# Performance work log

Measured on AMD Instinct MI355X. Metric: run time of the kernel, lower is better.

The kernel has to match this reference:

```python
import jax, jax.numpy as jnp
import numpy as np

N = 500000
D = 256
B = 1024  # number of graphs / segments


def setup_inputs() -> dict:
    key = jax.random.key(0)
    k1, k2, k3, k4 = jax.random.split(key, 4)
    x = jax.random.normal(k1, (N, D), dtype=jnp.float32)
    batch = jnp.sort(jax.random.randint(k2, (N,), 0, B))
    W1 = jax.random.normal(k3, (D, D // 2), dtype=jnp.float32) * (1.0 / np.sqrt(D))
    b1 = jnp.zeros((D // 2,), dtype=jnp.float32)
    W2 = jax.random.normal(k4, (D // 2, 1), dtype=jnp.float32) * (1.0 / np.sqrt(D // 2))
    b2 = jnp.zeros((1,), dtype=jnp.float32)
    return {"x": x, "batch": batch, "W1": W1, "b1": b1, "W2": W2, "b2": b2}


def _segment_mean(vals, seg, num_segments):
    # torch_scatter scatter_mean: sum / count (0 for empty segments)
    s = jax.ops.segment_sum(vals, seg, num_segments=num_segments)
    cnt = jax.ops.segment_sum(jnp.ones((vals.shape[0],), vals.dtype), seg,
                              num_segments=num_segments)
    return s / jnp.maximum(cnt, 1.0)[:, None]


def reference(x, batch, W1, b1, W2, b2):
    n = x.shape[0]
    # attention MLP -> (N, 1)
    h = jax.nn.relu(x @ W1 + b1)
    w = h @ W2 + b2
    # global max-shifted exp (as in source: w - w.max())
    w = jnp.exp(w - jnp.max(w))
    # denom = scatter_mean(w, batch)[batch] * N
    mean_w = _segment_mean(w, batch, B)            # (B, 1)
    denom = mean_w[batch] * jnp.float32(n)          # (N, 1)
    # pooled = scatter_mean(w * x / (denom + 1e-8), batch)
    pooled = _segment_mean(w * x / (denom + 1e-8), batch, B)  # (B, D)
    return pooled
```

## Files before the change

kernel.cpp:

```cpp
#include <hip/hip_runtime.h>
#include <math.h>

typedef float f32x4 __attribute__((ext_vector_type(4)));
typedef __attribute__((ext_vector_type(8))) _Float16 f16x8;
typedef __attribute__((ext_vector_type(4))) _Float16 f16x4;

#define DD 256
#define DH 128
#define NSPLIT 2
#define TROWS 64

__global__ void ap_setup(const float* __restrict__ W1, _Float16* __restrict__ w1f,
                         const int* __restrict__ batch, int* __restrict__ start,
                         int nrows, int bseg) {
  const int bid = blockIdx.x;
  if (bid < 16) {
    int t = bid * 256 + threadIdx.x;
    int l = t & 63;
    int tile = t >> 6;
    int kt = tile >> 3, nt = tile & 7;
    int kbase = kt * 32 + (l >> 4) * 8;
    int col = nt * 16 + (l & 15);
#pragma unroll
    for (int j = 0; j < 8; ++j) {
      w1f[t * 8 + j] = (_Float16)W1[(kbase + j) * DH + col];
    }
  } else {
    int i = (bid - 16) * 256 + threadIdx.x;
    if (i >= nrows) return;
    int c = batch[i];
    int p = (i == 0) ? -1 : batch[i - 1];
    for (int b = p + 1; b <= c; ++b) start[b] = i;
    if (i == nrows - 1) {
      for (int b = c + 1; b <= bseg; ++b) start[b] = nrows;
    }
  }
}

__global__ __launch_bounds__(512, 1)
void ap_fused(const float* __restrict__ x, const _Float16* __restrict__ w1f,
              const float* __restrict__ b1, const float* __restrict__ W2,
              const float* __restrict__ b2, const int* __restrict__ start,
              float* __restrict__ pooledPart, float* __restrict__ mPart,
              float* __restrict__ swPart, int nrows) {
  __shared__ __align__(16) _Float16 xsh[2][TROWS * 256];
  __shared__ float praw[2][4][TROWS];
  __shared__ float swArr[8];

  const int tid = threadIdx.x;
  const int wv = tid >> 6;
  const int np = wv & 3;
  const int rgp = wv >> 2;
  const int l = tid & 63;
  const int l15 = l & 15, lhi = l >> 4;

  const int bi = blockIdx.x;
  const int b = bi >> 1;
  const int q = bi & (NSPLIT - 1);
  const int s0 = start[b], e0 = start[b + 1];
  const int cnt = e0 - s0;
  const int L = (cnt + NSPLIT - 1) >> 1;
  const int s = s0 + q * L;
  int pe = s + L;
  if (pe > e0) pe = e0;
  const int e = pe;
  const int ce = (e > 0) ? (e - 1) : 0;

  f16x8 Breg[16];
#pragma unroll
  for (int kt = 0; kt < 8; ++kt) {
#pragma unroll
    for (int nt2 = 0; nt2 < 2; ++nt2) {
      Breg[kt * 2 + nt2] =
          *((const f16x8*)w1f + (size_t)(kt * 8 + np * 2 + nt2) * 64 + l);
    }
  }

  float b1f[2], w2f[2];
#pragma unroll
  for (int nt2 = 0; nt2 < 2; ++nt2) {
    const int idx = (np * 2 + nt2) * 16 + l15;
    b1f[nt2] = b1[idx];
    w2f[nt2] = W2[idx];
  }
  const float bb = *b2;
  const float NI = -__builtin_inff();

  f32x4 accp = {0.f, 0.f, 0.f, 0.f};
  float m = NI;
  float swv = 0.f;

  f32x4 xcol[8], xnext[8];
#pragma unroll
  for (int i = 0; i < 8; ++i) {
    int grow = s + wv * 8 + i;
    if (grow > ce) grow = ce;
    if (grow < 0) grow = 0;
    xcol[i] = *(const f32x4*)(x + (size_t)grow * DD + l * 4);
  }
#pragma unroll
  for (int i = 0; i < 8; ++i) {
    const int R = wv * 8 + i;
    const int gp = l ^ ((R & 7) << 1);
    f16x4 h4;
#pragma unroll
    for (int j = 0; j < 4; ++j) h4[j] = (_Float16)xcol[i][j];
    *(f16x4*)(xsh[0] + (size_t)(R * 64 + gp) * 4) = h4;
  }
  __syncthreads();

  int buf = 0;
  for (int t0 = s; t0 < e; t0 += TROWS) {
    const bool hasNext = (t0 + TROWS < e);

    if (hasNext) {
#pragma unroll
      for (int i = 0; i < 8; ++i) {
        int grow = t0 + TROWS + wv * 8 + i;
        if (grow > ce) grow = ce;
        xnext[i] = *(const f32x4*)(x + (size_t)grow * DD + l * 4);
      }
    }

    f32x4 acc[2][2];
#pragma unroll
    for (int rg2 = 0; rg2 < 2; ++rg2)
#pragma unroll
      for (int nt2 = 0; nt2 < 2; ++nt2) acc[rg2][nt2] = f32x4{0.f, 0.f, 0.f, 0.f};
#pragma unroll
    for (int kt = 0; kt < 8; ++kt) {
#pragma unroll
      for (int rg2 = 0; rg2 < 2; ++rg2) {
        const int Rr = rgp * 32 + rg2 * 16 + l15;
        const int gp = (kt * 8 + lhi * 2) ^ ((Rr & 7) << 1);
        const f16x8 ah = *(const f16x8*)(xsh[buf] + (size_t)(Rr * 64 + gp) * 4);
        acc[rg2][0] =
            __builtin_amdgcn_mfma_f32_16x16x32_f16(ah, Breg[kt * 2 + 0], acc[rg2][0], 0, 0, 0);
        acc[rg2][1] =
            __builtin_amdgcn_mfma_f32_16x16x32_f16(ah, Breg[kt * 2 + 1], acc[rg2][1], 0, 0, 0);
      }
    }

    float pr[2][4];
#pragma unroll
    for (int rg2 = 0; rg2 < 2; ++rg2) {
#pragma unroll
      for (int r = 0; r < 4; ++r) {
        float t = fmaxf(acc[rg2][0][r] + b1f[0], 0.f) * w2f[0] +
                  fmaxf(acc[rg2][1][r] + b1f[1], 0.f) * w2f[1];
        pr[rg2][r] = t;
      }
    }
#pragma unroll
    for (int mm = 1; mm < 16; mm <<= 1) {
#pragma unroll
      for (int rg2 = 0; rg2 < 2; ++rg2)
#pragma unroll
        for (int r = 0; r < 4; ++r) pr[rg2][r] += __shfl_xor(pr[rg2][r], mm, 64);
    }
    if (l15 == 0) {
#pragma unroll
      for (int rg2 = 0; rg2 < 2; ++rg2)
#pragma unroll
        for (int r = 0; r < 4; ++r)
          praw[buf][np][rgp * 32 + rg2 * 16 + lhi * 4 + r] = pr[rg2][r];
    }

    if (hasNext) {
#pragma unroll
      for (int i = 0; i < 8; ++i) {
        const int R = wv * 8 + i;
        const int gp = l ^ ((R & 7) << 1);
        f16x4 h4;
#pragma unroll
        for (int j = 0; j < 4; ++j) h4[j] = (_Float16)xnext[i][j];
        *(f16x4*)(xsh[buf ^ 1] + (size_t)(R * 64 + gp) * 4) = h4;
      }
    }

    __syncthreads();

    const float tot = (t0 + l < e)
                          ? (praw[buf][0][l] + praw[buf][1][l] +
                             praw[buf][2][l] + praw[buf][3][l] + bb)
                          : NI;
    float tv = tot;
#pragma unroll
    for (int mm = 1; mm < 64; mm <<= 1) tv = fmaxf(tv, __shfl_xor(tv, mm, 64));
    const float nm = fmaxf(m, tv);
    const float factor = expf(m - nm);
    m = nm;
    accp *= factor;
    swv *= factor;

#pragma unroll
    for (int i = 0; i < 8; ++i) {
      const int R = wv * 8 + i;
      const float wi = expf(__shfl(tot, R, 64) - m);
      swv += wi;
      accp += wi * xcol[i];
    }
#pragma unroll
    for (int i = 0; i < 8; ++i) xcol[i] = xnext[i];
    buf ^= 1;
  }

  __syncthreads();
  float* pooled = (float*)xsh;
  *(f32x4*)(pooled + (size_t)(wv * 256 + l * 4)) = accp;
  if (l == 0) swArr[wv] = swv;
  __syncthreads();
  if (tid < 64) {
    float sum_w = 0.f;
#pragma unroll
    for (int p = 0; p < 8; ++p) sum_w += swArr[p];
    const f32x4* pw = (const f32x4*)pooled;
    f32x4 v = ((pw[0 * 64 + tid] + pw[1 * 64 + tid]) +
               (pw[2 * 64 + tid] + pw[3 * 64 + tid]));
    f32x4 w = ((pw[4 * 64 + tid] + pw[5 * 64 + tid]) +
               (pw[6 * 64 + tid] + pw[7 * 64 + tid]));
    *(f32x4*)(pooledPart + (size_t)bi * DD + tid * 4) = v + w;
    if (tid == 0) { mPart[bi] = m; swPart[bi] = sum_w; }
  }
}

__global__ __launch_bounds__(64)
void ap_final(const float* __restrict__ pooledPart, const float* __restrict__ mPart,
              const float* __restrict__ swPart, const int* __restrict__ start,
              float* __restrict__ out, int nrows) {
  const int b = blockIdx.x;
  const int tid = threadIdx.x;
  const float NI = -__builtin_inff();
  float mq[NSPLIT];
#pragma unroll
  for (int qv = 0; qv < NSPLIT; ++qv) mq[qv] = mPart[b * NSPLIT + qv];
  float m_f = NI;
#pragma unroll
  for (int qv = 0; qv < NSPLIT; ++qv) m_f = fmaxf(m_f, mq[qv]);
  float fac[NSPLIT];
  float sum_w = 0.f;
#pragma unroll
  for (int qv = 0; qv < NSPLIT; ++qv) {
    fac[qv] = (mq[qv] == NI) ? 0.f : expf(mq[qv] - m_f);
    sum_w += swPart[b * NSPLIT + qv] * fac[qv];
  }
  const int cnt = start[b + 1] - start[b];
  const float cntf = (float)(cnt > 0 ? cnt : 1);
  const float scale = 1.0f / (((sum_w / cntf) * (float)nrows + 1e-8f) * cntf);
  f32x4 r = f32x4{0.f, 0.f, 0.f, 0.f};
#pragma unroll
  for (int qv = 0; qv < NSPLIT; ++qv) {
    r += ((const f32x4*)(pooledPart + (size_t)(b * NSPLIT + qv) * DD))[tid] * fac[qv];
  }
  r *= scale;
  *(f32x4*)(out + (size_t)b * DD + tid * 4) = r;
}

extern "C" void kernel_launch(void* const* d_in, const int* in_sizes, int n_in,
                              void* d_out, int out_size, void* d_ws, size_t ws_size,
                              hipStream_t stream) {
  const float* x     = (const float*)d_in[0];
  const int*   batch = (const int*)d_in[1];
  const float* W1    = (const float*)d_in[2];
  const float* b1    = (const float*)d_in[3];
  const float* W2    = (const float*)d_in[4];
  const float* b2    = (const float*)d_in[5];
  float* out = (float*)d_out;

  const int nrows = in_sizes[1];
  const int bseg = out_size / DD;

  float* pooledPart = (float*)d_ws;
  float* mPart  = pooledPart + (size_t)bseg * NSPLIT * DD;
  float* swPart = mPart + bseg * NSPLIT;
  _Float16* w1f = (_Float16*)(swPart + bseg * NSPLIT);
  int* start = (int*)(w1f + 64 * 64 * 8);

  ap_setup<<<16 + (nrows + 255) / 256, 256, 0, stream>>>(W1, w1f, batch, start,
                                                         nrows, bseg);
  ap_fused<<<bseg * NSPLIT, 512, 0, stream>>>(x, w1f, b1, W2, b2, start,
                                              pooledPart, mPart, swPart, nrows);
  ap_final<<<bseg, 64, 0, stream>>>(pooledPart, mPart, swPart, start, out, nrows);
}
```

Measured before the change: 152.9 us.

## Halve row tile to 32 and repartition MFMA work across 8 column waves

Shrinks the per-iteration row tile from 64 to 32 rows and gives each of the 8 waves one 16-column slice of the hidden layer instead of a 4×2 row/column split. Each wave now holds fewer W1 fragments, accumulators and prefetched x rows, and launch bounds ask for 2 blocks per CU. The aim is higher occupancy to hide global-load latency. In exchange there are twice as many loop iterations and barriers, and a larger cross-wave reduction of 8 partial scores per row.

New measurement: 145.9 us. -4.6%, faster.

```diff
diff --git a/kernel.cpp b/kernel.cpp
--- a/kernel.cpp
+++ b/kernel.cpp
@@ -8,7 +8,7 @@
 #define DD 256
 #define DH 128
 #define NSPLIT 2
-#define TROWS 64
+#define TROWS 32
 
 __global__ void ap_setup(const float* __restrict__ W1, _Float16* __restrict__ w1f,
                          const int* __restrict__ batch, int* __restrict__ start,
@@ -37,20 +37,18 @@
   }
 }
 
-__global__ __launch_bounds__(512, 1)
+__global__ __launch_bounds__(512, 2)
 void ap_fused(const float* __restrict__ x, const _Float16* __restrict__ w1f,
               const float* __restrict__ b1, const float* __restrict__ W2,
               const float* __restrict__ b2, const int* __restrict__ start,
               float* __restrict__ pooledPart, float* __restrict__ mPart,
               float* __restrict__ swPart, int nrows) {
   __shared__ __align__(16) _Float16 xsh[2][TROWS * 256];
-  __shared__ float praw[2][4][TROWS];
+  __shared__ float praw[2][8][TROWS];
   __shared__ float swArr[8];
 
   const int tid = threadIdx.x;
   const int wv = tid >> 6;
-  const int np = wv & 3;
-  const int rgp = wv >> 2;
   const int l = tid & 63;
   const int l15 = l & 15, lhi = l >> 4;
 
@@ -66,23 +64,13 @@
   const int e = pe;
   const int ce = (e > 0) ? (e - 1) : 0;
 
-  f16x8 Breg[16];
+  f16x8 Breg[8];
 #pragma unroll
   for (int kt = 0; kt < 8; ++kt) {
-#pragma unroll
-    for (int nt2 = 0; nt2 < 2; ++nt2) {
-      Breg[kt * 2 + nt2] =
-          *((const f16x8*)w1f + (size_t)(kt * 8 + np * 2 + nt2) * 64 + l);
-    }
-  }
-
-  float b1f[2], w2f[2];
-#pragma unroll
-  for (int nt2 = 0; nt2 < 2; ++nt2) {
-    const int idx = (np * 2 + nt2) * 16 + l15;
-    b1f[nt2] = b1[idx];
-    w2f[nt2] = W2[idx];
-  }
+    Breg[kt] = *((const f16x8*)w1f + (size_t)(kt * 8 + wv) * 64 + l);
+  }
+  const float b1f = b1[wv * 16 + l15];
+  const float w2f = W2[wv * 16 + l15];
   const float bb = *b2;
   const float NI = -__builtin_inff();
 
@@ -90,17 +78,17 @@
   float m = NI;
   float swv = 0.f;
 
-  f32x4 xcol[8], xnext[8];
-#pragma unroll
-  for (int i = 0; i < 8; ++i) {
-    int grow = s + wv * 8 + i;
+  f32x4 xcol[4], xnext[4];
+#pragma unroll
+  for (int i = 0; i < 4; ++i) {
+    int grow = s + wv * 4 + i;
     if (grow > ce) grow = ce;
     if (grow < 0) grow = 0;
     xcol[i] = *(const f32x4*)(x + (size_t)grow * DD + l * 4);
   }
 #pragma unroll
-  for (int i = 0; i < 8; ++i) {
-    const int R = wv * 8 + i;
+  for (int i = 0; i < 4; ++i) {
+    const int R = wv * 4 + i;
     const int gp = l ^ ((R & 7) << 1);
     f16x4 h4;
 #pragma unroll
@@ -115,42 +103,34 @@
 
     if (hasNext) {
 #pragma unroll
-      for (int i = 0; i < 8; ++i) {
-        int grow = t0 + TROWS + wv * 8 + i;
+      for (int i = 0; i < 4; ++i) {
+        int grow = t0 + TROWS + wv * 4 + i;
         if (grow > ce) grow = ce;
         xnext[i] = *(const f32x4*)(x + (size_t)grow * DD + l * 4);
       }
     }
 
-    f32x4 acc[2][2];
-#pragma unroll
-    for (int rg2 = 0; rg2 < 2; ++rg2)
-#pragma unroll
-      for (int nt2 = 0; nt2 < 2; ++nt2) acc[rg2][nt2] = f32x4{0.f, 0.f, 0.f, 0.f};
+    f32x4 acc[2];
+#pragma unroll
+    for (int rg2 = 0; rg2 < 2; ++rg2) acc[rg2] = f32x4{0.f, 0.f, 0.f, 0.f};
 #pragma unroll
     for (int kt = 0; kt < 8; ++kt) {
 #pragma unroll
       for (int rg2 = 0; rg2 < 2; ++rg2) {
-        const int Rr = rgp * 32 + rg2 * 16 + l15;
+        const int Rr = rg2 * 16 + l15;
         const int gp = (kt * 8 + lhi * 2) ^ ((Rr & 7) << 1);
         const f16x8 ah = *(const f16x8*)(xsh[buf] + (size_t)(Rr * 64 + gp) * 4);
-        acc[rg2][0] =
-            __builtin_amdgcn_mfma_f32_16x16x32_f16(ah, Breg[kt * 2 + 0], acc[rg2][0], 0, 0, 0);
-        acc[rg2][1] =
-            __builtin_amdgcn_mfma_f32_16x16x32_f16(ah, Breg[kt * 2 + 1], acc[rg2][1], 0, 0, 0);
+        acc[rg2] =
+            __builtin_amdgcn_mfma_f32_16x16x32_f16(ah, Breg[kt], acc[rg2], 0, 0, 0);
       }
     }
 
     float pr[2][4];
 #pragma unroll
-    for (int rg2 = 0; rg2 < 2; ++rg2) {
-#pragma unroll
-      for (int r = 0; r < 4; ++r) {
-        float t = fmaxf(acc[rg2][0][r] + b1f[0], 0.f) * w2f[0] +
-                  fmaxf(acc[rg2][1][r] + b1f[1], 0.f) * w2f[1];
-        pr[rg2][r] = t;
-      }
-    }
+    for (int rg2 = 0; rg2 < 2; ++rg2)
+#pragma unroll
+      for (int r = 0; r < 4; ++r)
+        pr[rg2][r] = fmaxf(acc[rg2][r] + b1f, 0.f) * w2f;
 #pragma unroll
     for (int mm = 1; mm < 16; mm <<= 1) {
 #pragma unroll
@@ -163,13 +143,13 @@
       for (int rg2 = 0; rg2 < 2; ++rg2)
 #pragma unroll
         for (int r = 0; r < 4; ++r)
-          praw[buf][np][rgp * 32 + rg2 * 16 + lhi * 4 + r] = pr[rg2][r];
+          praw[buf][wv][rg2 * 16 + lhi * 4 + r] = pr[rg2][r];
     }
 
     if (hasNext) {
 #pragma unroll
-      for (int i = 0; i < 8; ++i) {
-        const int R = wv * 8 + i;
+      for (int i = 0; i < 4; ++i) {
+        const int R = wv * 4 + i;
         const int gp = l ^ ((R & 7) << 1);
         f16x4 h4;
 #pragma unroll
@@ -180,10 +160,13 @@
 
     __syncthreads();
 
-    const float tot = (t0 + l < e)
-                          ? (praw[buf][0][l] + praw[buf][1][l] +
-                             praw[buf][2][l] + praw[buf][3][l] + bb)
-                          : NI;
+    const int lr = l & 31;
+    float tot = NI;
+    if (t0 + lr < e) {
+      tot = bb;
+#pragma unroll
+      for (int p = 0; p < 8; ++p) tot += praw[buf][p][lr];
+    }
     float tv = tot;
 #pragma unroll
     for (int mm = 1; mm < 64; mm <<= 1) tv = fmaxf(tv, __shfl_xor(tv, mm, 64));
@@ -194,14 +177,14 @@
     swv *= factor;
 
 #pragma unroll
-    for (int i = 0; i < 8; ++i) {
-      const int R = wv * 8 + i;
+    for (int i = 0; i < 4; ++i) {
+      const int R = wv * 4 + i;
       const float wi = expf(__shfl(tot, R, 64) - m);
       swv += wi;
       accp += wi * xcol[i];
     }
 #pragma unroll
-    for (int i = 0; i < 8; ++i) xcol[i] = xnext[i];
+    for (int i = 0; i < 4; ++i) xcol[i] = xnext[i];
     buf ^= 1;
   }
 
```
